# Kernel optimization log

Hardware: AMD Instinct MI355X
Metric: run time of the kernel (lower is better)

The kernel has to match this reference:

```python
import jax, jax.numpy as jnp
import numpy as np

B, L, D = 8, 1024, 512
H, DK, DV = 8, 64, 64
EPS = 1e-6
NEG = -1e9


def setup_inputs() -> dict:
    key = jax.random.key(0)
    ks = jax.random.split(key, 12)
    def xavier(k, shape):
        fan_out, fan_in = shape
        bound = float(np.sqrt(6.0 / (fan_in + fan_out)))
        return jax.random.uniform(k, shape, jnp.float32, -bound, bound)
    return {
        "q": jax.random.normal(ks[0], (B, L, D), jnp.float32),
        "k": jax.random.normal(ks[1], (B, L, D), jnp.float32),
        "v": jax.random.normal(ks[2], (B, L, D), jnp.float32),
        "event_type": jax.random.randint(ks[3], (B, L), 0, 2, jnp.int32),
        "mask": jax.random.randint(ks[4], (B, L, L), 0, 2, jnp.int32).astype(bool),
        "w_qs": xavier(ks[5], (H * DK, D)),
        "w_ex_en_qs": xavier(ks[6], (H * DK, D)),
        "w_ks": xavier(ks[7], (H * DK, D)),
        "w_vs": xavier(ks[8], (H * DV, D)),
        "w_fc": xavier(ks[9], (D, H * DV)),
        "b_fc": jnp.zeros((D,), jnp.float32),
        "ln_gamma": jnp.ones((D,), jnp.float32),
        "ln_beta": jnp.zeros((D,), jnp.float32),
    }


def _layer_norm(x, gamma, beta):
    mu = jnp.mean(x, axis=-1, keepdims=True)
    var = jnp.var(x, axis=-1, keepdims=True)
    return (x - mu) * jax.lax.rsqrt(var + EPS) * gamma + beta


def reference(q, k, v, event_type, mask, w_qs, w_ex_en_qs, w_ks, w_vs, w_fc, b_fc, ln_gamma, ln_beta):
    residual = q
    qn = _layer_norm(q, ln_gamma, ln_beta)  # normalize_before=True

    # event-type flags: en_en = prev is en AND present is en; ex_en = prev is ex AND present is en
    is_en = event_type != 0                                   # [B, L]
    en_en = (is_en[:, :, None] & is_en[:, None, :])[:, None]  # [B, 1, L, L]
    ex_en = ((~is_en)[:, :, None] & is_en[:, None, :])[:, None]

    def proj(x, w, d):  # torch Linear: x @ w.T, then split heads -> [B, H, L, d]
        return (x @ w.T).reshape(B, L, H, d).transpose(0, 2, 1, 3)

    q_en = proj(qn, w_qs, DK)
    q_ex = proj(qn, w_ex_en_qs, DK)
    kh = proj(k, w_ks, DK)
    vh = proj(v, w_vs, DV)

    temp = jnp.asarray(DK ** 0.5, qn.dtype)
    scores_en = jnp.einsum('bhqd,bhkd->bhqk', q_en / temp, kh)
    scores_en = jnp.where(mask[:, None], NEG, scores_en)      # masked branch
    scores_ex = jnp.einsum('bhqd,bhkd->bhqk', q_ex / temp, kh)  # unmasked branch

    blended = en_en * scores_en + ex_en * scores_ex           # [B, H, L, L]
    attn = jax.nn.softmax(blended, axis=-1)

    out = jnp.einsum('bhqk,bhkd->bhqd', attn, vh)             # PV
    out = out.transpose(0, 2, 1, 3).reshape(B, L, H * DV)
    out = out @ w_fc.T + b_fc
    out = out + residual
    return out, attn
```

## Files before the change

kernel.cpp:

```cpp
#include <hip/hip_runtime.h>

typedef __attribute__((ext_vector_type(8))) short bf16x8;
typedef __attribute__((ext_vector_type(4))) float f32x4;

#define DEVI static __device__ __forceinline__

constexpr float NEGV = -1e9f;

DEVI unsigned short f2b(float f) {
  union { float f; unsigned int u; } c; c.f = f;
  unsigned int lsb = (c.u >> 16) & 1u;
  return (unsigned short)((c.u + 0x7fffu + lsb) >> 16);
}

DEVI void gload16(const unsigned short* g, unsigned short* l) {
  __builtin_amdgcn_global_load_lds(
      (const __attribute__((address_space(1))) unsigned int*)g,
      (__attribute__((address_space(3))) unsigned int*)l, 16, 0, 0);
}

__global__ void mask_detect(const unsigned int* __restrict__ m, int n, int* flag) {
  unsigned int v = 0;
  for (int i = blockIdx.x * blockDim.x + threadIdx.x; i < n; i += gridDim.x * blockDim.x)
    v |= m[i];
  if (v & ~1u) atomicOr(flag, 1);
}

__global__ void mask_canon_bits(const void* __restrict__ mraw, unsigned int* __restrict__ mb,
                                int nwords, const int* __restrict__ flag) {
  int i = blockIdx.x * blockDim.x + threadIdx.x;
  if (i >= nwords) return;
  bool isbytes = (*flag != 0);
  unsigned int out = 0;
  if (isbytes) {
    const unsigned int* p = (const unsigned int*)mraw + (size_t)i * 8;
    #pragma unroll
    for (int w = 0; w < 8; w++) {
      unsigned int bw = p[w];
      out |= ((bw & 1u) << (w * 4)) | (((bw >> 8) & 1u) << (w * 4 + 1)) |
             (((bw >> 16) & 1u) << (w * 4 + 2)) | (((bw >> 24) & 1u) << (w * 4 + 3));
    }
  } else {
    const int4* p = (const int4*)mraw + (size_t)i * 8;
    #pragma unroll
    for (int w = 0; w < 8; w++) {
      int4 v = p[w];
      out |= ((v.x != 0 ? 1u : 0u) << (w * 4)) | ((v.y != 0 ? 1u : 0u) << (w * 4 + 1)) |
             ((v.z != 0 ? 1u : 0u) << (w * 4 + 2)) | ((v.w != 0 ? 1u : 0u) << (w * 4 + 3));
    }
  }
  mb[i] = out;
}

__global__ __launch_bounds__(256) void ln_kernel(const float* __restrict__ q,
    const float* __restrict__ gamma, const float* __restrict__ beta,
    unsigned short* __restrict__ qn) {
  int row = blockIdx.x;
  int t = threadIdx.x;
  const float* x = q + (size_t)row * 512;
  float2 v = reinterpret_cast<const float2*>(x)[t];
  float s = v.x + v.y, s2 = v.x * v.x + v.y * v.y;
  #pragma unroll
  for (int o = 32; o; o >>= 1) { s += __shfl_xor(s, o); s2 += __shfl_xor(s2, o); }
  __shared__ float ls[4], ls2[4];
  int w = t >> 6;
  if ((t & 63) == 0) { ls[w] = s; ls2[w] = s2; }
  __syncthreads();
  float S = ls[0] + ls[1] + ls[2] + ls[3];
  float S2 = ls2[0] + ls2[1] + ls2[2] + ls2[3];
  float mu = S * (1.f / 512.f);
  float var = S2 * (1.f / 512.f) - mu * mu;
  float r = rsqrtf(var + 1e-6f);
  float g0 = gamma[t * 2], g1 = gamma[t * 2 + 1];
  float b0 = beta[t * 2], b1 = beta[t * 2 + 1];
  ushort2 o;
  o.x = f2b((v.x - mu) * r * g0 + b0);
  o.y = f2b((v.y - mu) * r * g1 + b1);
  reinterpret_cast<ushort2*>(qn + (size_t)row * 512)[t] = o;
}

template<int MODE, bool CVX, bool CVW>
__global__ __launch_bounds__(256) void gemm_bt(
    const void* __restrict__ Xv,
    const void* __restrict__ Wv,
    void* __restrict__ Yv,
    float scale,
    const float* __restrict__ bias,
    const float* __restrict__ resid) {
  constexpr int LDT = 40;
  __shared__ __align__(16) unsigned short lA[64 * LDT];
  __shared__ __align__(16) unsigned short lB[64 * LDT];
  int t = threadIdx.x;
  int w = t >> 6, l = t & 63, lr = l & 15, lg = l >> 4;
  int mb = blockIdx.x * 64, nb = blockIdx.y * 64;
  f32x4 acc[4];
  #pragma unroll
  for (int n = 0; n < 4; n++) acc[n] = {0.f, 0.f, 0.f, 0.f};
  int sr = t >> 2, sc = (t & 3) * 8;
  for (int k0 = 0; k0 < 512; k0 += 32) {
    __syncthreads();
    if constexpr (CVX) {
      const float* src = (const float*)Xv + (size_t)(mb + sr) * 512 + k0 + sc;
      float4 x0 = *reinterpret_cast<const float4*>(src);
      float4 x1 = *reinterpret_cast<const float4*>(src + 4);
      ushort4 h0{f2b(x0.x), f2b(x0.y), f2b(x0.z), f2b(x0.w)};
      ushort4 h1{f2b(x1.x), f2b(x1.y), f2b(x1.z), f2b(x1.w)};
      *reinterpret_cast<ushort4*>(&lA[sr * LDT + sc]) = h0;
      *reinterpret_cast<ushort4*>(&lA[sr * LDT + sc + 4]) = h1;
    } else {
      *reinterpret_cast<float4*>(&lA[sr * LDT + sc]) =
          *reinterpret_cast<const float4*>((const unsigned short*)Xv + (size_t)(mb + sr) * 512 + k0 + sc);
    }
    if constexpr (CVW) {
      const float* src = (const float*)Wv + (size_t)(nb + sr) * 512 + k0 + sc;
      float4 x0 = *reinterpret_cast<const float4*>(src);
      float4 x1 = *reinterpret_cast<const float4*>(src + 4);
      ushort4 h0{f2b(x0.x), f2b(x0.y), f2b(x0.z), f2b(x0.w)};
      ushort4 h1{f2b(x1.x), f2b(x1.y), f2b(x1.z), f2b(x1.w)};
      *reinterpret_cast<ushort4*>(&lB[sr * LDT + sc]) = h0;
      *reinterpret_cast<ushort4*>(&lB[sr * LDT + sc + 4]) = h1;
    } else {
      *reinterpret_cast<float4*>(&lB[sr * LDT + sc]) =
          *reinterpret_cast<const float4*>((const unsigned short*)Wv + (size_t)(nb + sr) * 512 + k0 + sc);
    }
    __syncthreads();
    bf16x8 a = *reinterpret_cast<const bf16x8*>(&lA[(w * 16 + lr) * LDT + lg * 8]);
    #pragma unroll
    for (int n = 0; n < 4; n++) {
      bf16x8 bb = *reinterpret_cast<const bf16x8*>(&lB[(n * 16 + lr) * LDT + lg * 8]);
      acc[n] = __builtin_amdgcn_mfma_f32_16x16x32_bf16(a, bb, acc[n], 0, 0, 0);
    }
  }
  #pragma unroll
  for (int n = 0; n < 4; n++) {
    #pragma unroll
    for (int j = 0; j < 4; j++) {
      int m = mb + w * 16 + lg * 4 + j;
      int c = nb + n * 16 + lr;
      float val = acc[n][j] * scale;
      if constexpr (MODE == 0) {
        reinterpret_cast<unsigned short*>(Yv)[(size_t)m * 512 + c] = f2b(val);
      } else if constexpr (MODE == 1) {
        int bb_ = m >> 10, ll = m & 1023, hh = c >> 6, dd = c & 63;
        reinterpret_cast<unsigned short*>(Yv)[((size_t)((bb_ * 8 + hh) * 64 + dd)) * 1024 + ll] = f2b(val);
      } else {
        reinterpret_cast<float*>(Yv)[(size_t)m * 512 + c] =
            val + bias[c] + resid[(size_t)m * 512 + c];
      }
    }
  }
}

__global__ __launch_bounds__(256) void attn_kernel(
    const unsigned short* __restrict__ qen,
    const unsigned short* __restrict__ qex,
    const unsigned short* __restrict__ kh,
    const unsigned short* __restrict__ vhT,
    const int* __restrict__ etype,
    const unsigned int* __restrict__ mbits,
    float* __restrict__ attn_g,
    unsigned short* __restrict__ pv_out) {
  int qt = blockIdx.x, h = blockIdx.y, b = blockIdx.z;
  int t = threadIdx.x, w = t >> 6, l = t & 63, lr = l & 15, lg = l >> 4;
  __shared__ unsigned int ekbits[32];
  __shared__ unsigned int mkill[64 * 33];
  __shared__ __align__(16) unsigned short klds[2][2048];
  __shared__ __align__(16) unsigned short vlds[2][2048];
  __shared__ __align__(16) unsigned short pbuf[4][16][40];

  int qb = qt * 64 + w * 16;
  int qrowA = qb + lr;
  bool evA = etype[b * 1024 + qrowA] != 0;
  const unsigned short* qp = evA ? qen : qex;
  size_t qoff = (size_t)(b * 1024 + qrowA) * 512 + h * 64;
  bf16x8 a0 = *reinterpret_cast<const bf16x8*>(qp + qoff + lg * 8);
  bf16x8 a1 = *reinterpret_cast<const bf16x8*>(qp + qoff + 32 + lg * 8);

  if (t < 32) {
    unsigned int wdd = 0;
    const int4* ep = (const int4*)(etype + b * 1024 + t * 32);
    #pragma unroll
    for (int j4 = 0; j4 < 8; j4++) {
      int4 e = ep[j4];
      wdd |= ((e.x != 0 ? 1u : 0u) << (j4 * 4)) | ((e.y != 0 ? 1u : 0u) << (j4 * 4 + 1)) |
             ((e.z != 0 ? 1u : 0u) << (j4 * 4 + 2)) | ((e.w != 0 ? 1u : 0u) << (j4 * 4 + 3));
    }
    ekbits[t] = wdd;
  }
  {
    const unsigned int* mslice = mbits + ((size_t)(b * 1024 + qt * 64)) * 32;
    for (int i = t; i < 2048; i += 256) {
      int row = i >> 5, wd = i & 31;
      bool evq_row = etype[b * 1024 + qt * 64 + row] != 0;
      mkill[row * 33 + wd] = evq_row ? mslice[i] : 0u;
    }
  }

  int qrc[4], qlc[4];
  #pragma unroll
  for (int j = 0; j < 4; j++) { qlc[j] = w * 16 + lg * 4 + j; qrc[j] = qt * 64 + qlc[j]; }

  int srow = t >> 3, sb8 = t & 7;
  const unsigned short* kgsrc = kh + ((size_t)(b * 1024) + srow) * 512 + h * 64
                                + ((sb8 ^ (srow & 7)) << 3);
  unsigned short* kdst0 = &klds[0][(t & 192) * 8];
  unsigned short* kdst1 = &klds[1][(t & 192) * 8];
  int vrow = t >> 2, vb4 = t & 3;
  const unsigned short* vb_base = vhT + ((size_t)((b * 8 + h) * 64)) * 1024;
  const unsigned short* vgsrc = vb_base + (size_t)vrow * 1024 + ((vb4 ^ ((vrow >> 1) & 3)) << 3);
  unsigned short* vdst0 = &vlds[0][(t & 192) * 8];
  unsigned short* vdst1 = &vlds[1][(t & 192) * 8];

  gload16(kgsrc, kdst0);
  __syncthreads();

  float srun[4] = {0.f, 0.f, 0.f, 0.f};
  for (int c = 0; c < 32; c++) {
    int cur = c & 1;
    if (c < 31) gload16(kgsrc + (size_t)(c + 1) * 32 * 512, cur ? kdst0 : kdst1);
    #pragma unroll
    for (int c2 = 0; c2 < 2; c2++) {
      int kt = c * 2 + c2;
      int row = c2 * 16 + lr, r7 = row & 7;
      bf16x8 b0 = *reinterpret_cast<const bf16x8*>(&klds[cur][row * 64 + ((lg ^ r7) << 3)]);
      bf16x8 b1 = *reinterpret_cast<const bf16x8*>(&klds[cur][row * 64 + (((4 + lg) ^ r7) << 3)]);
      f32x4 cc = {0.f, 0.f, 0.f, 0.f};
      cc = __builtin_amdgcn_mfma_f32_16x16x32_bf16(a0, b0, cc, 0, 0, 0);
      cc = __builtin_amdgcn_mfma_f32_16x16x32_bf16(a1, b1, cc, 0, 0, 0);
      int wcol = kt >> 1, bitpos = ((kt & 1) << 4) + lr;
      bool ekb = (ekbits[wcol] >> bitpos) & 1;
      #pragma unroll
      for (int j = 0; j < 4; j++) {
        bool mk = (mkill[qlc[j] * 33 + wcol] >> bitpos) & 1;
        float val = ekb ? (mk ? NEGV : cc[j]) : 0.f;
        srun[j] += __expf(val);
      }
    }
    __syncthreads();
  }
  float rS[4];
  #pragma unroll
  for (int j = 0; j < 4; j++) {
    float s = srun[j];
    s += __shfl_xor(s, 1); s += __shfl_xor(s, 2);
    s += __shfl_xor(s, 4); s += __shfl_xor(s, 8);
    rS[j] = 1.f / s;
  }

  f32x4 oacc[4];
  #pragma unroll
  for (int n = 0; n < 4; n++) oacc[n] = {0.f, 0.f, 0.f, 0.f};
  float* ag = attn_g + ((size_t)(b * 8 + h)) * 1024 * 1024;

  gload16(kgsrc, kdst0);
  gload16(vgsrc, vdst0);
  __syncthreads();

  for (int c = 0; c < 32; c++) {
    int cur = c & 1;
    if (c < 31) {
      gload16(kgsrc + (size_t)(c + 1) * 32 * 512, cur ? kdst0 : kdst1);
      gload16(vgsrc + (size_t)(c + 1) * 32, cur ? vdst0 : vdst1);
    }
    #pragma unroll
    for (int c2 = 0; c2 < 2; c2++) {
      int kt = c * 2 + c2;
      int row = c2 * 16 + lr, r7 = row & 7;
      bf16x8 b0 = *reinterpret_cast<const bf16x8*>(&klds[cur][row * 64 + ((lg ^ r7) << 3)]);
      bf16x8 b1 = *reinterpret_cast<const bf16x8*>(&klds[cur][row * 64 + (((4 + lg) ^ r7) << 3)]);
      f32x4 cc = {0.f, 0.f, 0.f, 0.f};
      cc = __builtin_amdgcn_mfma_f32_16x16x32_bf16(a0, b0, cc, 0, 0, 0);
      cc = __builtin_amdgcn_mfma_f32_16x16x32_bf16(a1, b1, cc, 0, 0, 0);
      int wcol = kt >> 1, bitpos = ((kt & 1) << 4) + lr;
      bool ekb = (ekbits[wcol] >> bitpos) & 1;
      int kidx = kt * 16 + lr;
      #pragma unroll
      for (int j = 0; j < 4; j++) {
        bool mk = (mkill[qlc[j] * 33 + wcol] >> bitpos) & 1;
        float val = ekb ? (mk ? NEGV : cc[j]) : 0.f;
        float p = __expf(val) * rS[j];
        __builtin_nontemporal_store(p, &ag[(size_t)qrc[j] * 1024 + kidx]);
        pbuf[w][lg * 4 + j][(kt & 1) * 16 + lr] = f2b(p);
      }
      if (kt & 1) {
        bf16x8 pa = *reinterpret_cast<const bf16x8*>(&pbuf[w][lr][lg * 8]);
        #pragma unroll
        for (int n = 0; n < 4; n++) {
          int vr = n * 16 + lr;
          int cb = (lg ^ ((vr >> 1) & 3)) << 3;
          bf16x8 vb = *reinterpret_cast<const bf16x8*>(&vlds[cur][vr * 32 + cb]);
          oacc[n] = __builtin_amdgcn_mfma_f32_16x16x32_bf16(pa, vb, oacc[n], 0, 0, 0);
        }
      }
    }
    __syncthreads();
  }
  #pragma unroll
  for (int n = 0; n < 4; n++) {
    #pragma unroll
    for (int j = 0; j < 4; j++) {
      __builtin_nontemporal_store(f2b(oacc[n][j]),
          &pv_out[(size_t)(b * 1024 + qrc[j]) * 512 + h * 64 + n * 16 + lr]);
    }
  }
}

extern "C" void kernel_launch(void* const* d_in, const int* in_sizes, int n_in,
                              void* d_out, int out_size, void* d_ws, size_t ws_size,
                              hipStream_t stream) {
  (void)in_sizes; (void)n_in; (void)out_size; (void)ws_size;
  const float* q     = (const float*)d_in[0];
  const float* k     = (const float*)d_in[1];
  const float* v     = (const float*)d_in[2];
  const int* etype   = (const int*)d_in[3];
  const void* mask_raw = d_in[4];
  const float* w_qs  = (const float*)d_in[5];
  const float* w_ex  = (const float*)d_in[6];
  const float* w_ks  = (const float*)d_in[7];
  const float* w_vs  = (const float*)d_in[8];
  const float* w_fc  = (const float*)d_in[9];
  const float* b_fc  = (const float*)d_in[10];
  const float* gamma = (const float*)d_in[11];
  const float* beta  = (const float*)d_in[12];

  char* ws = (char*)d_ws;
  const size_t MB = 1024 * 1024;
  unsigned short* qn   = (unsigned short*)(ws);
  unsigned short* qen  = (unsigned short*)(ws + 8 * MB);
  unsigned short* qex  = (unsigned short*)(ws + 16 * MB);
  unsigned short* khb  = (unsigned short*)(ws + 24 * MB);
  unsigned short* vhT  = (unsigned short*)(ws + 32 * MB);
  unsigned short* ao   = (unsigned short*)(ws + 40 * MB);
  unsigned int* mbits  = (unsigned int*)(ws + 48 * MB);
  int* mflag           = (int*)(ws + 49 * MB);

  float* outp = (float*)d_out;
  float* attn_g = outp + (size_t)8 * 1024 * 512;

  ln_kernel<<<8192, 256, 0, stream>>>(q, gamma, beta, qn);

  const int MASK_N = 8 * 1024 * 1024;
  hipMemsetAsync(mflag, 0, 4, stream);
  mask_detect<<<2048, 256, 0, stream>>>((const unsigned int*)mask_raw, MASK_N / 4, mflag);
  const int NWORDS = MASK_N / 32;
  mask_canon_bits<<<(NWORDS + 255) / 256, 256, 0, stream>>>(mask_raw, mbits, NWORDS, mflag);

  dim3 gg(128, 8);
  gemm_bt<0, false, true><<<gg, 256, 0, stream>>>(qn, w_qs, qen, 0.125f, nullptr, nullptr);
  gemm_bt<0, false, true><<<gg, 256, 0, stream>>>(qn, w_ex, qex, 0.125f, nullptr, nullptr);
  gemm_bt<0, true,  true><<<gg, 256, 0, stream>>>(k,  w_ks, khb, 1.0f, nullptr, nullptr);
  gemm_bt<1, true,  true><<<gg, 256, 0, stream>>>(v,  w_vs, vhT, 1.0f, nullptr, nullptr);

  attn_kernel<<<dim3(16, 8, 8), 256, 0, stream>>>(qen, qex, khb, vhT, etype, mbits,
                                                  attn_g, ao);

  gemm_bt<2, false, true><<<gg, 256, 0, stream>>>(ao, w_fc, outp, 1.0f, b_fc, q);
}
```

Measured before the change: 261.3 us.

## Deepen attention K/V prefetch pipeline, vectorize attn stores, remap blocks across XCDs

The attention kernel now uses four-slot LDS ring buffers for K and V, prefetching two chunks ahead. Per-chunk __syncthreads are replaced by explicit s_waitcnt vmcnt counts plus s_barrier, so global loads overlap with compute. The probability matrix is now written as 16-byte vector stores taken from the bf16-rounded P tile instead of scalar fp32 stores. This reduces store instruction count but makes the returned attn values bf16-precision. Blocks are also remapped from a 1D grid so each XCD handles a fixed set of (batch, head) groups, for better L2 reuse of K/V.

New measurement: 309.6 us. +18.5%, slower.

```diff
diff --git a/kernel.cpp b/kernel.cpp
--- a/kernel.cpp
+++ b/kernel.cpp
@@ -12,12 +12,19 @@
   unsigned int lsb = (c.u >> 16) & 1u;
   return (unsigned short)((c.u + 0x7fffu + lsb) >> 16);
 }
+DEVI float sb2f(short s) {
+  union { unsigned int u; float f; } c;
+  c.u = ((unsigned int)(unsigned short)s) << 16;
+  return c.f;
+}
 
 DEVI void gload16(const unsigned short* g, unsigned short* l) {
   __builtin_amdgcn_global_load_lds(
       (const __attribute__((address_space(1))) unsigned int*)g,
       (__attribute__((address_space(3))) unsigned int*)l, 16, 0, 0);
 }
+
+#define CHUNK_SYNC(N) asm volatile("s_waitcnt vmcnt(" #N ") lgkmcnt(0)\n\ts_barrier" ::: "memory")
 
 __global__ void mask_detect(const unsigned int* __restrict__ m, int n, int* flag) {
   unsigned int v = 0;
@@ -160,12 +167,17 @@
     const unsigned int* __restrict__ mbits,
     float* __restrict__ attn_g,
     unsigned short* __restrict__ pv_out) {
-  int qt = blockIdx.x, h = blockIdx.y, b = blockIdx.z;
+  int lid = blockIdx.x;
+  int xcd = lid & 7, slot = lid >> 3;
+  int qt = slot & 15;
+  int g = ((slot >> 4) << 3) | xcd;
+  int h = g & 7, b = g >> 3;
+
   int t = threadIdx.x, w = t >> 6, l = t & 63, lr = l & 15, lg = l >> 4;
   __shared__ unsigned int ekbits[32];
   __shared__ unsigned int mkill[64 * 33];
-  __shared__ __align__(16) unsigned short klds[2][2048];
-  __shared__ __align__(16) unsigned short vlds[2][2048];
+  __shared__ __align__(16) unsigned short klds[4][2048];
+  __shared__ __align__(16) unsigned short vlds[4][2048];
   __shared__ __align__(16) unsigned short pbuf[4][16][40];
 
   int qb = qt * 64 + w * 16;
@@ -203,42 +215,90 @@
   int srow = t >> 3, sb8 = t & 7;
   const unsigned short* kgsrc = kh + ((size_t)(b * 1024) + srow) * 512 + h * 64
                                 + ((sb8 ^ (srow & 7)) << 3);
-  unsigned short* kdst0 = &klds[0][(t & 192) * 8];
-  unsigned short* kdst1 = &klds[1][(t & 192) * 8];
   int vrow = t >> 2, vb4 = t & 3;
   const unsigned short* vb_base = vhT + ((size_t)((b * 8 + h) * 64)) * 1024;
   const unsigned short* vgsrc = vb_base + (size_t)vrow * 1024 + ((vb4 ^ ((vrow >> 1) & 3)) << 3);
-  unsigned short* vdst0 = &vlds[0][(t & 192) * 8];
-  unsigned short* vdst1 = &vlds[1][(t & 192) * 8];
-
-  gload16(kgsrc, kdst0);
-  __syncthreads();
+  int wofs = (t & 192) * 8;
 
   float srun[4] = {0.f, 0.f, 0.f, 0.f};
-  for (int c = 0; c < 32; c++) {
-    int cur = c & 1;
-    if (c < 31) gload16(kgsrc + (size_t)(c + 1) * 32 * 512, cur ? kdst0 : kdst1);
-    #pragma unroll
-    for (int c2 = 0; c2 < 2; c2++) {
-      int kt = c * 2 + c2;
+  float rS[4];
+  f32x4 oacc[4];
+  #pragma unroll
+  for (int n = 0; n < 4; n++) oacc[n] = {0.f, 0.f, 0.f, 0.f};
+  float* ag = attn_g + ((size_t)(b * 8 + h)) * 1024 * 1024;
+  float* agrow = ag + (size_t)(qb + lr) * 1024 + lg * 8;
+
+  auto computeP1 = [&](int c) {
+    int kb = c & 3;
+    #pragma unroll
+    for (int c2 = 0; c2 < 2; ++c2) {
       int row = c2 * 16 + lr, r7 = row & 7;
-      bf16x8 b0 = *reinterpret_cast<const bf16x8*>(&klds[cur][row * 64 + ((lg ^ r7) << 3)]);
-      bf16x8 b1 = *reinterpret_cast<const bf16x8*>(&klds[cur][row * 64 + (((4 + lg) ^ r7) << 3)]);
+      bf16x8 b0 = *reinterpret_cast<const bf16x8*>(&klds[kb][row * 64 + ((lg ^ r7) << 3)]);
+      bf16x8 b1 = *reinterpret_cast<const bf16x8*>(&klds[kb][row * 64 + (((4 + lg) ^ r7) << 3)]);
       f32x4 cc = {0.f, 0.f, 0.f, 0.f};
       cc = __builtin_amdgcn_mfma_f32_16x16x32_bf16(a0, b0, cc, 0, 0, 0);
       cc = __builtin_amdgcn_mfma_f32_16x16x32_bf16(a1, b1, cc, 0, 0, 0);
-      int wcol = kt >> 1, bitpos = ((kt & 1) << 4) + lr;
-      bool ekb = (ekbits[wcol] >> bitpos) & 1;
+      int bitpos = (c2 << 4) + lr;
+      bool ekb = (ekbits[c] >> bitpos) & 1;
       #pragma unroll
       for (int j = 0; j < 4; j++) {
-        bool mk = (mkill[qlc[j] * 33 + wcol] >> bitpos) & 1;
+        bool mk = (mkill[qlc[j] * 33 + c] >> bitpos) & 1;
         float val = ekb ? (mk ? NEGV : cc[j]) : 0.f;
         srun[j] += __expf(val);
       }
     }
-    __syncthreads();
-  }
-  float rS[4];
+  };
+
+  auto computeP2 = [&](int c) {
+    int kb = c & 3;
+    #pragma unroll
+    for (int c2 = 0; c2 < 2; ++c2) {
+      int row = c2 * 16 + lr, r7 = row & 7;
+      bf16x8 b0 = *reinterpret_cast<const bf16x8*>(&klds[kb][row * 64 + ((lg ^ r7) << 3)]);
+      bf16x8 b1 = *reinterpret_cast<const bf16x8*>(&klds[kb][row * 64 + (((4 + lg) ^ r7) << 3)]);
+      f32x4 cc = {0.f, 0.f, 0.f, 0.f};
+      cc = __builtin_amdgcn_mfma_f32_16x16x32_bf16(a0, b0, cc, 0, 0, 0);
+      cc = __builtin_amdgcn_mfma_f32_16x16x32_bf16(a1, b1, cc, 0, 0, 0);
+      int bitpos = (c2 << 4) + lr;
+      bool ekb = (ekbits[c] >> bitpos) & 1;
+      #pragma unroll
+      for (int j = 0; j < 4; j++) {
+        bool mk = (mkill[qlc[j] * 33 + c] >> bitpos) & 1;
+        float val = ekb ? (mk ? NEGV : cc[j]) : 0.f;
+        float p = __expf(val) * rS[j];
+        pbuf[w][lg * 4 + j][(c2 << 4) + lr] = f2b(p);
+      }
+      if (c2) {
+        bf16x8 pa = *reinterpret_cast<const bf16x8*>(&pbuf[w][lr][lg * 8]);
+        f32x4 f0, f1;
+        f0[0] = sb2f(pa[0]); f0[1] = sb2f(pa[1]); f0[2] = sb2f(pa[2]); f0[3] = sb2f(pa[3]);
+        f1[0] = sb2f(pa[4]); f1[1] = sb2f(pa[5]); f1[2] = sb2f(pa[6]); f1[3] = sb2f(pa[7]);
+        __builtin_nontemporal_store(f0, reinterpret_cast<f32x4*>(agrow + c * 32));
+        __builtin_nontemporal_store(f1, reinterpret_cast<f32x4*>(agrow + c * 32 + 4));
+        #pragma unroll
+        for (int n = 0; n < 4; n++) {
+          int vr = n * 16 + lr;
+          int cb = (lg ^ ((vr >> 1) & 3)) << 3;
+          bf16x8 vb = *reinterpret_cast<const bf16x8*>(&vlds[kb][vr * 32 + cb]);
+          oacc[n] = __builtin_amdgcn_mfma_f32_16x16x32_bf16(pa, vb, oacc[n], 0, 0, 0);
+        }
+      }
+    }
+  };
+
+  gload16(kgsrc, &klds[0][wofs]);
+  gload16(kgsrc + (size_t)32 * 512, &klds[1][wofs]);
+  gload16(kgsrc + (size_t)64 * 512, &klds[2][wofs]);
+  CHUNK_SYNC(2);
+  computeP1(0);
+  for (int c = 1; c < 30; ++c) {
+    gload16(kgsrc + (size_t)(c + 2) * 32 * 512, &klds[(c + 2) & 3][wofs]);
+    CHUNK_SYNC(2);
+    computeP1(c);
+  }
+  CHUNK_SYNC(1); computeP1(30);
+  CHUNK_SYNC(0); computeP1(31);
+
   #pragma unroll
   for (int j = 0; j < 4; j++) {
     float s = srun[j];
@@ -247,54 +307,24 @@
     rS[j] = 1.f / s;
   }
 
-  f32x4 oacc[4];
-  #pragma unroll
-  for (int n = 0; n < 4; n++) oacc[n] = {0.f, 0.f, 0.f, 0.f};
-  float* ag = attn_g + ((size_t)(b * 8 + h)) * 1024 * 1024;
-
-  gload16(kgsrc, kdst0);
-  gload16(vgsrc, vdst0);
-  __syncthreads();
-
-  for (int c = 0; c < 32; c++) {
-    int cur = c & 1;
-    if (c < 31) {
-      gload16(kgsrc + (size_t)(c + 1) * 32 * 512, cur ? kdst0 : kdst1);
-      gload16(vgsrc + (size_t)(c + 1) * 32, cur ? vdst0 : vdst1);
-    }
-    #pragma unroll
-    for (int c2 = 0; c2 < 2; c2++) {
-      int kt = c * 2 + c2;
-      int row = c2 * 16 + lr, r7 = row & 7;
-      bf16x8 b0 = *reinterpret_cast<const bf16x8*>(&klds[cur][row * 64 + ((lg ^ r7) << 3)]);
-      bf16x8 b1 = *reinterpret_cast<const bf16x8*>(&klds[cur][row * 64 + (((4 + lg) ^ r7) << 3)]);
-      f32x4 cc = {0.f, 0.f, 0.f, 0.f};
-      cc = __builtin_amdgcn_mfma_f32_16x16x32_bf16(a0, b0, cc, 0, 0, 0);
-      cc = __builtin_amdgcn_mfma_f32_16x16x32_bf16(a1, b1, cc, 0, 0, 0);
-      int wcol = kt >> 1, bitpos = ((kt & 1) << 4) + lr;
-      bool ekb = (ekbits[wcol] >> bitpos) & 1;
-      int kidx = kt * 16 + lr;
-      #pragma unroll
-      for (int j = 0; j < 4; j++) {
-        bool mk = (mkill[qlc[j] * 33 + wcol] >> bitpos) & 1;
-        float val = ekb ? (mk ? NEGV : cc[j]) : 0.f;
-        float p = __expf(val) * rS[j];
-        __builtin_nontemporal_store(p, &ag[(size_t)qrc[j] * 1024 + kidx]);
-        pbuf[w][lg * 4 + j][(kt & 1) * 16 + lr] = f2b(p);
-      }
-      if (kt & 1) {
-        bf16x8 pa = *reinterpret_cast<const bf16x8*>(&pbuf[w][lr][lg * 8]);
-        #pragma unroll
-        for (int n = 0; n < 4; n++) {
-          int vr = n * 16 + lr;
-          int cb = (lg ^ ((vr >> 1) & 3)) << 3;
-          bf16x8 vb = *reinterpret_cast<const bf16x8*>(&vlds[cur][vr * 32 + cb]);
-          oacc[n] = __builtin_amdgcn_mfma_f32_16x16x32_bf16(pa, vb, oacc[n], 0, 0, 0);
-        }
-      }
-    }
-    __syncthreads();
-  }
+  gload16(kgsrc, &klds[0][wofs]);
+  gload16(vgsrc, &vlds[0][wofs]);
+  gload16(kgsrc + (size_t)32 * 512, &klds[1][wofs]);
+  gload16(vgsrc + 32, &vlds[1][wofs]);
+
+  gload16(kgsrc + (size_t)64 * 512, &klds[2][wofs]);
+  gload16(vgsrc + 64, &vlds[2][wofs]);
+  CHUNK_SYNC(4);
+  computeP2(0);
+  for (int c = 1; c < 30; ++c) {
+    gload16(kgsrc + (size_t)(c + 2) * 32 * 512, &klds[(c + 2) & 3][wofs]);
+    gload16(vgsrc + (size_t)(c + 2) * 32, &vlds[(c + 2) & 3][wofs]);
+    CHUNK_SYNC(6);
+    computeP2(c);
+  }
+  CHUNK_SYNC(4); computeP2(30);
+  CHUNK_SYNC(4); computeP2(31);
+
   #pragma unroll
   for (int n = 0; n < 4; n++) {
     #pragma unroll
@@ -351,8 +381,8 @@
   gemm_bt<0, true,  true><<<gg, 256, 0, stream>>>(k,  w_ks, khb, 1.0f, nullptr, nullptr);
   gemm_bt<1, true,  true><<<gg, 256, 0, stream>>>(v,  w_vs, vhT, 1.0f, nullptr, nullptr);
 
-  attn_kernel<<<dim3(16, 8, 8), 256, 0, stream>>>(qen, qex, khb, vhT, etype, mbits,
-                                                  attn_g, ao);
+  attn_kernel<<<dim3(1024), 256, 0, stream>>>(qen, qex, khb, vhT, etype, mbits,
+                                              attn_g, ao);
 
   gemm_bt<2, false, true><<<gg, 256, 0, stream>>>(ao, w_fc, outp, 1.0f, b_fc, q);
 }
```
